# Kernel optimization log

Measured on AMD Instinct MI355X. Metric: run time of the kernel, lower is better.

The kernel has to match this reference:

```python
import jax, jax.numpy as jnp
import numpy as np

N, E = 20000, 320000          # nodes, edges (avg degree 16)
IN, OUT, EC = 256, 256, 64    # in_channels == out_channels (required by BN placement)
BN_EPS = 1e-5


def setup_inputs() -> dict:
    key = jax.random.key(0)
    ks = jax.random.split(key, 8)
    def lin(k, fan_in, fan_out):
        # kaiming-uniform-ish init like nn.Linear
        bound = 1.0 / np.sqrt(fan_in)
        return jax.random.uniform(k, (fan_in, fan_out), jnp.float32, -bound, bound)
    return {
        "x": jax.random.normal(ks[0], (N, IN), jnp.float32),
        "edge_index": jax.random.randint(ks[1], (2, E), 0, N),
        "edge_attr": jax.random.normal(ks[2], (E, EC), jnp.float32),
        "W_edge": lin(ks[3], EC, IN),          # edge_lin (no bias)
        "W_rel": lin(ks[4], IN, OUT),           # GraphConv lin_rel weight
        "b_rel": jnp.zeros((OUT,), jnp.float32),  # GraphConv lin_rel bias
        "W_root": lin(ks[5], IN, OUT),          # GraphConv lin_root (no bias)
        "gamma": jnp.ones((OUT,), jnp.float32),  # BN weight
        "beta": jnp.zeros((OUT,), jnp.float32),  # BN bias
        "W_res": lin(ks[6], IN, OUT),           # res_lin (no bias)
    }


def reference(x, edge_index, edge_attr, W_edge, W_rel, b_rel, W_root, gamma, beta, W_res):
    src, dst = edge_index[0], edge_index[1]
    # edge feature projection: [E, EC] -> [E, IN]
    e = edge_attr @ W_edge
    # message passing: gather source node feats, modulate by edge feats, scatter-add to dst
    msg = x[src] * e                                   # [E, IN]
    agg = jax.ops.segment_sum(msg, dst, num_segments=x.shape[0])  # [N, IN]
    # GraphConv: lin_rel(aggregate) + lin_root(x)
    h = agg @ W_rel + b_rel + x @ W_root               # [N, OUT]
    h = jax.nn.relu(h)
    # BatchNorm1d (training mode: batch statistics over nodes)
    mean = h.mean(axis=0)
    var = ((h - mean) ** 2).mean(axis=0)
    h = (h - mean) * jax.lax.rsqrt(var + BN_EPS) * gamma + beta
    # residual branch
    return h + x @ W_res
```

## Files before the change

kernel.cpp:

```cpp
#include <hip/hip_runtime.h>
#include <hip/hip_bf16.h>


#define N_NODES 20000
#define E_EDGES 320000
#define C 256
#define CE 64
#define MAXDEG 64
#define BN_EPS 1e-5f

typedef __attribute__((ext_vector_type(8))) short short8;
typedef __attribute__((ext_vector_type(8))) unsigned short ushort8;
typedef __attribute__((ext_vector_type(4))) float f32x4;
typedef __attribute__((ext_vector_type(4))) unsigned short ushort4v;

static __device__ __forceinline__ float bf2f(unsigned short u) {
    union { unsigned int i; float f; } v; v.i = (unsigned int)u << 16; return v.f;
}
static __device__ __forceinline__ unsigned short f2bf(float f) {
    __hip_bfloat16 h = __float2bfloat16(f);
    return *reinterpret_cast<unsigned short*>(&h);
}

__global__ __launch_bounds__(256) void k_wprep(
    const float* __restrict__ W_rel, const float* __restrict__ W_root,
    const float* __restrict__ W_res, const float* __restrict__ W_edge,
    unsigned short* __restrict__ wt_hi, unsigned short* __restrict__ wte_hi) {
    int b = blockIdx.x, n = threadIdx.x;
    if (b < 768) {
        int m = b >> 8, k = b & 255;
        const float* W = (m == 0) ? W_rel : (m == 1) ? W_root : W_res;
        size_t o = (((size_t)m * 16 + (n >> 4)) * 8 + (k >> 5)) * 512
                 + (size_t)(((n & 15) | (((k >> 3) & 3) << 4)) * 8) + (k & 7);
        wt_hi[o] = f2bf(W[k * C + n]);
    } else {
        int k = b - 768;
        size_t o = ((size_t)(n >> 4) * 2 + (k >> 5)) * 512
                 + (size_t)(((n & 15) | (((k >> 3) & 3) << 4)) * 8) + (k & 7);
        wte_hi[o] = f2bf(W_edge[k * C + n]);
    }
}

__global__ void k_bucket(const int* __restrict__ ei, int* __restrict__ deg,
                         int2* __restrict__ elist2) {
    int e = blockIdx.x * blockDim.x + threadIdx.x;
    if (e < E_EDGES) {
        int d = ei[E_EDGES + e];
        int s = ei[e];
        int slot = atomicAdd(&deg[d], 1);
        if (slot < MAXDEG) elist2[d * MAXDEG + slot] = make_int2(e, s);
    }
}

__global__ __launch_bounds__(256, 4) void k_fusedagg(
    const float* __restrict__ x, const float* __restrict__ ea,
    const unsigned short* __restrict__ wte_hi,
    const int* __restrict__ deg, const int2* __restrict__ elist2,
    float* __restrict__ agg) {
    __shared__ short lds[16384];
    __shared__ int es[MAXDEG], ss[MAXDEG];
    const int tid = threadIdx.x;
    const int node = blockIdx.x;

    int dr = deg[node];
    const int d = dr < MAXDEG ? dr : MAXDEG;
    if (d == 0) {
        agg[(size_t)node * C + tid] = 0.f;
        return;
    }
    if (tid < d) {
        int2 p = elist2[node * MAXDEG + tid];
        es[tid] = p.x; ss[tid] = p.y;
    }
    __syncthreads();

    const int rtmax = (d + 15) >> 4;

#pragma unroll
    for (int i = 0; i < 4; ++i) {
        int f = tid + 256 * i;
        int r = f >> 4, k4 = (f & 15) * 4;
        if (r < rtmax * 16) {
            float4 v = {0.f, 0.f, 0.f, 0.f};
            if (r < d)
                v = *reinterpret_cast<const float4*>(&ea[(size_t)es[r] * CE + k4]);
            unsigned short h0 = f2bf(v.x), h1 = f2bf(v.y), h2 = f2bf(v.z), h3 = f2bf(v.w);
            ushort4v hv = {h0, h1, h2, h3};
            ushort4v lv = {f2bf(v.x - bf2f(h0)), f2bf(v.y - bf2f(h1)),
                           f2bf(v.z - bf2f(h2)), f2bf(v.w - bf2f(h3))};
            int rt = r >> 4, ks = k4 >> 5;
            int lane = (r & 15) | (((k4 >> 3) & 3) << 4);
            int base = (((rt * 2 + ks) * 2 + 0) * 64 + lane) * 8 + (k4 & 7);
            *reinterpret_cast<ushort4v*>(&lds[base]) = hv;
            *reinterpret_cast<ushort4v*>(&lds[base + 512]) = lv;
        }
    }
    __syncthreads();

    const int w = tid >> 6, l = tid & 63;
    f32x4 acc[2][4];
#pragma unroll
    for (int rt = 0; rt < 2; ++rt)
#pragma unroll
        for (int ct = 0; ct < 4; ++ct) acc[rt][ct] = (f32x4){0.f, 0.f, 0.f, 0.f};
    const int rtc = rtmax < 2 ? rtmax : 2;

#pragma unroll
    for (int ks = 0; ks < 2; ++ks) {
        short8 b[4];
#pragma unroll
        for (int ct = 0; ct < 4; ++ct) {
            int nt = w * 4 + ct;
            b[ct] = *reinterpret_cast<const short8*>(&wte_hi[(size_t)(nt * 2 + ks) * 512 + l * 8]);
        }
        for (int rt = 0; rt < rtc; ++rt) {
            int base = ((rt * 2 + ks) * 2) * 512 + l * 8;
            short8 ah = *reinterpret_cast<const short8*>(&lds[base]);
            short8 al = *reinterpret_cast<const short8*>(&lds[base + 512]);
#pragma unroll
            for (int ct = 0; ct < 4; ++ct) {
                acc[rt][ct] = __builtin_amdgcn_mfma_f32_16x16x32_bf16(ah, b[ct], acc[rt][ct], 0, 0, 0);
                acc[rt][ct] = __builtin_amdgcn_mfma_f32_16x16x32_bf16(al, b[ct], acc[rt][ct], 0, 0, 0);
            }
        }
    }

    f32x4 acc3[2][4];
    const bool deep = (rtmax > 2);
    if (deep) {
#pragma unroll
        for (int rt = 0; rt < 2; ++rt)
#pragma unroll
            for (int ct = 0; ct < 4; ++ct) acc3[rt][ct] = (f32x4){0.f, 0.f, 0.f, 0.f};
#pragma unroll
        for (int ks = 0; ks < 2; ++ks) {
            short8 b[4];
#pragma unroll
            for (int ct = 0; ct < 4; ++ct) {
                int nt = w * 4 + ct;
                b[ct] = *reinterpret_cast<const short8*>(&wte_hi[(size_t)(nt * 2 + ks) * 512 + l * 8]);
            }
            for (int rt = 2; rt < rtmax; ++rt) {
                int base = ((rt * 2 + ks) * 2) * 512 + l * 8;
                short8 ah = *reinterpret_cast<const short8*>(&lds[base]);
                short8 al = *reinterpret_cast<const short8*>(&lds[base + 512]);
#pragma unroll
                for (int ct = 0; ct < 4; ++ct) {
                    acc3[rt - 2][ct] = __builtin_amdgcn_mfma_f32_16x16x32_bf16(ah, b[ct], acc3[rt - 2][ct], 0, 0, 0);
                    acc3[rt - 2][ct] = __builtin_amdgcn_mfma_f32_16x16x32_bf16(al, b[ct], acc3[rt - 2][ct], 0, 0, 0);
                }
            }
        }
    }

    __syncthreads();
    for (int rt = 0; rt < rtc; ++rt)
#pragma unroll
        for (int ct = 0; ct < 4; ++ct) {
            int col = w * 64 + ct * 16 + (l & 15);
#pragma unroll
            for (int q = 0; q < 4; ++q) {
                int r = rt * 16 + (l >> 4) * 4 + q;
                lds[r * C + col] = (short)f2bf(acc[rt][ct][q]);
            }
        }
    if (deep) {
        for (int rt = 2; rt < rtmax; ++rt)
#pragma unroll
            for (int ct = 0; ct < 4; ++ct) {
                int col = w * 64 + ct * 16 + (l & 15);
#pragma unroll
                for (int q = 0; q < 4; ++q) {
                    int r = rt * 16 + (l >> 4) * 4 + q;
                    lds[r * C + col] = (short)f2bf(acc3[rt - 2][ct][q]);
                }
            }
    }
    __syncthreads();

    const int c = tid;
    float accv = 0.f;
    for (int i = 0; i < d; i += 4) {
        int m = d - i;
        float xv[4], ev[4];
#pragma unroll
        for (int j = 0; j < 4; ++j) {
            if (j < m) {
                xv[j] = x[(size_t)ss[i + j] * C + c];
                ev[j] = bf2f((unsigned short)lds[(i + j) * C + c]);
            } else { xv[j] = 0.f; ev[j] = 0.f; }
        }
#pragma unroll
        for (int j = 0; j < 4; ++j) accv += ev[j] * xv[j];
    }
    agg[(size_t)node * C + c] = accv;
}

__global__ __launch_bounds__(256, 4) void k_gemm(
    const float* __restrict__ aggt, const float* __restrict__ x,
    const unsigned short* __restrict__ wt_hi,
    float* __restrict__ g_rel, float* __restrict__ g_root,
    float* __restrict__ g_res) {
    __shared__ short AB[16384];
    const int tid = threadIdx.x;
    const int n0 = blockIdx.x * 32;
    const int mat = blockIdx.y;
    const float* Asrc = (mat == 0) ? aggt : x;
    float* dst = (mat == 0) ? g_rel : (mat == 1) ? g_root : g_res;

#pragma unroll
    for (int i = 0; i < 8; ++i) {
        int f = tid + 256 * i;
        int r = f >> 6, k4 = (f & 63) * 4;
        float4 v = *reinterpret_cast<const float4*>(&Asrc[(size_t)(n0 + r) * C + k4]);
        unsigned short h0 = f2bf(v.x), h1 = f2bf(v.y), h2 = f2bf(v.z), h3 = f2bf(v.w);
        ushort4v hv = {h0, h1, h2, h3};
        ushort4v lv = {f2bf(v.x - bf2f(h0)), f2bf(v.y - bf2f(h1)),
                       f2bf(v.z - bf2f(h2)), f2bf(v.w - bf2f(h3))};
        int rt = r >> 4, ks = k4 >> 5;
        int lane = (r & 15) | (((k4 >> 3) & 3) << 4);
        int base = (((rt * 8 + ks) * 2 + 0) * 64 + lane) * 8 + (k4 & 7);
        *reinterpret_cast<ushort4v*>(&AB[base]) = hv;
        *reinterpret_cast<ushort4v*>(&AB[base + 512]) = lv;
    }
    __syncthreads();

    const int w = tid >> 6, l = tid & 63;
    f32x4 acc[2][4];
#pragma unroll
    for (int rt = 0; rt < 2; ++rt)
#pragma unroll
        for (int ct = 0; ct < 4; ++ct) acc[rt][ct] = (f32x4){0.f, 0.f, 0.f, 0.f};

    const unsigned short* wbase = wt_hi + (size_t)mat * 16 * 8 * 512;

#pragma unroll
    for (int ks = 0; ks < 8; ++ks) {
        short8 b[4];
#pragma unroll
        for (int ct = 0; ct < 4; ++ct) {
            int nt = w * 4 + ct;
            b[ct] = *reinterpret_cast<const short8*>(&wbase[(size_t)(nt * 8 + ks) * 512 + l * 8]);
        }
        short8 ah[2], al[2];
#pragma unroll
        for (int rt = 0; rt < 2; ++rt) {
            int base = ((rt * 8 + ks) * 2) * 512 + l * 8;
            ah[rt] = *reinterpret_cast<const short8*>(&AB[base]);
            al[rt] = *reinterpret_cast<const short8*>(&AB[base + 512]);
        }
#pragma unroll
        for (int ct = 0; ct < 4; ++ct)
#pragma unroll
            for (int rt = 0; rt < 2; ++rt) {
                acc[rt][ct] = __builtin_amdgcn_mfma_f32_16x16x32_bf16(ah[rt], b[ct], acc[rt][ct], 0, 0, 0);
                acc[rt][ct] = __builtin_amdgcn_mfma_f32_16x16x32_bf16(al[rt], b[ct], acc[rt][ct], 0, 0, 0);
            }
    }

#pragma unroll
    for (int ct = 0; ct < 4; ++ct) {
        int col = w * 64 + ct * 16 + (l & 15);
#pragma unroll
        for (int rt = 0; rt < 2; ++rt)
#pragma unroll
            for (int q = 0; q < 4; ++q) {
                int node = n0 + rt * 16 + (l >> 4) * 4 + q;
                dst[(size_t)node * C + col] = acc[rt][ct][q];
            }
    }
}

__global__ __launch_bounds__(256) void k_bnstat(
    const float* __restrict__ g_rel, const float* __restrict__ g_root,
    const float* __restrict__ b_rel, float* __restrict__ chsum,
    float* __restrict__ chsumsq) {
    __shared__ float2 red[4 * 256];
    const int tid = threadIdx.x;
    const int c0 = (tid & 63) * 4, rg = tid >> 6;
    const int base = blockIdx.x * 32;
    float4 b4 = *reinterpret_cast<const float4*>(&b_rel[c0]);
    float4 s1 = {0.f, 0.f, 0.f, 0.f}, s2 = {0.f, 0.f, 0.f, 0.f};
#pragma unroll
    for (int i = 0; i < 8; ++i) {
        size_t row = (size_t)(base + rg * 8 + i) * C + c0;
        float4 hr = *reinterpret_cast<const float4*>(&g_rel[row]);
        float4 ho = *reinterpret_cast<const float4*>(&g_root[row]);
        float4 h;
        h.x = fmaxf(hr.x + ho.x + b4.x, 0.f);
        h.y = fmaxf(hr.y + ho.y + b4.y, 0.f);
        h.z = fmaxf(hr.z + ho.z + b4.z, 0.f);
        h.w = fmaxf(hr.w + ho.w + b4.w, 0.f);
        s1.x += h.x; s1.y += h.y; s1.z += h.z; s1.w += h.w;
        s2.x += h.x * h.x; s2.y += h.y * h.y;
        s2.z += h.z * h.z; s2.w += h.w * h.w;
    }
    red[rg * 256 + c0 + 0] = make_float2(s1.x, s2.x);
    red[rg * 256 + c0 + 1] = make_float2(s1.y, s2.y);
    red[rg * 256 + c0 + 2] = make_float2(s1.z, s2.z);
    red[rg * 256 + c0 + 3] = make_float2(s1.w, s2.w);
    __syncthreads();
    float a = 0.f, bsum = 0.f;
#pragma unroll
    for (int g = 0; g < 4; ++g) {
        float2 v = red[g * 256 + tid];
        a += v.x; bsum += v.y;
    }
    atomicAdd(&chsum[tid], a);
    atomicAdd(&chsumsq[tid], bsum);
}

__global__ __launch_bounds__(256) void k_finalize(
    const float* __restrict__ g_rel, const float* __restrict__ g_root,
    const float* __restrict__ b_rel, const float* __restrict__ chsum,
    const float* __restrict__ chsumsq, const float* __restrict__ gamma,
    const float* __restrict__ beta, float* out) {
    const float invN = 1.f / (float)N_NODES;
    int i = (blockIdx.x * blockDim.x + threadIdx.x) * 4;
    if (i >= N_NODES * C) return;
    int c = i & (C - 1);
    float4 hr = *reinterpret_cast<const float4*>(&g_rel[i]);
    float4 ho = *reinterpret_cast<const float4*>(&g_root[i]);
    float4 b4 = *reinterpret_cast<const float4*>(&b_rel[c]);
    float4 rv = *reinterpret_cast<const float4*>(&out[i]);
    float4 o;
    {
        float h = fmaxf(hr.x + ho.x + b4.x, 0.f);
        float m = chsum[c + 0] * invN;
        float v = chsumsq[c + 0] * invN - m * m;
        o.x = (h - m) * rsqrtf(v + BN_EPS) * gamma[c + 0] + beta[c + 0] + rv.x;
    }
    {
        float h = fmaxf(hr.y + ho.y + b4.y, 0.f);
        float m = chsum[c + 1] * invN;
        float v = chsumsq[c + 1] * invN - m * m;
        o.y = (h - m) * rsqrtf(v + BN_EPS) * gamma[c + 1] + beta[c + 1] + rv.y;
    }
    {
        float h = fmaxf(hr.z + ho.z + b4.z, 0.f);
        float m = chsum[c + 2] * invN;
        float v = chsumsq[c + 2] * invN - m * m;
        o.z = (h - m) * rsqrtf(v + BN_EPS) * gamma[c + 2] + beta[c + 2] + rv.z;
    }
    {
        float h = fmaxf(hr.w + ho.w + b4.w, 0.f);
        float m = chsum[c + 3] * invN;
        float v = chsumsq[c + 3] * invN - m * m;
        o.w = (h - m) * rsqrtf(v + BN_EPS) * gamma[c + 3] + beta[c + 3] + rv.w;
    }
    *reinterpret_cast<float4*>(&out[i]) = o;
}

extern "C" void kernel_launch(void* const* d_in, const int* in_sizes, int n_in,
                              void* d_out, int out_size, void* d_ws, size_t ws_size,
                              hipStream_t stream) {
    const float* x      = (const float*)d_in[0];
    const int*   ei     = (const int*)  d_in[1];
    const float* ea     = (const float*)d_in[2];
    const float* W_edge = (const float*)d_in[3];
    const float* W_rel  = (const float*)d_in[4];
    const float* b_rel  = (const float*)d_in[5];
    const float* W_root = (const float*)d_in[6];
    const float* gamma  = (const float*)d_in[7];
    const float* beta   = (const float*)d_in[8];
    const float* W_res  = (const float*)d_in[9];
    float* out = (float*)d_out;

    float* ws      = (float*)d_ws;
    float* aggt    = ws;
    float* chsum   = ws + (size_t)N_NODES * C;
    float* chsumsq = chsum + C;
    int*   deg     = (int*)(chsumsq + C);
    int2*  elist2  = (int2*)(deg + N_NODES);
    float* g_rel   = (float*)(elist2 + (size_t)N_NODES * MAXDEG);
    float* g_root  = g_rel + (size_t)N_NODES * C;
    unsigned short* wte_hi = (unsigned short*)(g_root + (size_t)N_NODES * C);
    unsigned short* wt_hi  = wte_hi + C * CE;
    size_t need = (char*)(wt_hi + 3 * C * C) - (char*)d_ws;
    if (ws_size < need) return;

    hipMemsetAsync(chsum, 0, 2 * C * sizeof(float) + N_NODES * sizeof(int), stream);

    k_wprep<<<832, 256, 0, stream>>>(W_rel, W_root, W_res, W_edge, wt_hi, wte_hi);
    k_bucket<<<(E_EDGES + 255) / 256, 256, 0, stream>>>(ei, deg, elist2);
    k_fusedagg<<<N_NODES, 256, 0, stream>>>(x, ea, wte_hi, deg, elist2, aggt);
    k_gemm<<<dim3(N_NODES / 32, 3), 256, 0, stream>>>(aggt, x, wt_hi,
                                                      g_rel, g_root, out);
    k_bnstat<<<N_NODES / 32, 256, 0, stream>>>(g_rel, g_root, b_rel, chsum, chsumsq);
    k_finalize<<<(N_NODES * C / 4 + 255) / 256, 256, 0, stream>>>(
        g_rel, g_root, b_rel, chsum, chsumsq, gamma, beta, out);
}
```

Before: 354.3 us.

## Pack two destination nodes per block in fused aggregation and swizzle LDS

The fused edge-projection/aggregation kernel now handles two destination nodes per block. Their edge lists are concatenated into one MFMA tile when the combined degree fits in 64 rows, otherwise the nodes are processed in two passes. This fills more of each 16-row MFMA tile, which previously held about one node's 16 edges, and halves the block count. It also XOR-swizzles the bf16 edge-feature staging buffer in LDS to reduce bank conflicts, at the cost of extra syncs and branching per pass.

```diff
diff --git a/kernel.cpp b/kernel.cpp
--- a/kernel.cpp
+++ b/kernel.cpp
@@ -60,78 +60,58 @@
     __shared__ short lds[16384];
     __shared__ int es[MAXDEG], ss[MAXDEG];
     const int tid = threadIdx.x;
-    const int node = blockIdx.x;
-
-    int dr = deg[node];
-    const int d = dr < MAXDEG ? dr : MAXDEG;
-    if (d == 0) {
-        agg[(size_t)node * C + tid] = 0.f;
-        return;
-    }
-    if (tid < d) {
-        int2 p = elist2[node * MAXDEG + tid];
-        es[tid] = p.x; ss[tid] = p.y;
-    }
-    __syncthreads();
-
-    const int rtmax = (d + 15) >> 4;
-
-#pragma unroll
-    for (int i = 0; i < 4; ++i) {
-        int f = tid + 256 * i;
-        int r = f >> 4, k4 = (f & 15) * 4;
-        if (r < rtmax * 16) {
-            float4 v = {0.f, 0.f, 0.f, 0.f};
-            if (r < d)
-                v = *reinterpret_cast<const float4*>(&ea[(size_t)es[r] * CE + k4]);
-            unsigned short h0 = f2bf(v.x), h1 = f2bf(v.y), h2 = f2bf(v.z), h3 = f2bf(v.w);
-            ushort4v hv = {h0, h1, h2, h3};
-            ushort4v lv = {f2bf(v.x - bf2f(h0)), f2bf(v.y - bf2f(h1)),
-                           f2bf(v.z - bf2f(h2)), f2bf(v.w - bf2f(h3))};
-            int rt = r >> 4, ks = k4 >> 5;
-            int lane = (r & 15) | (((k4 >> 3) & 3) << 4);
-            int base = (((rt * 2 + ks) * 2 + 0) * 64 + lane) * 8 + (k4 & 7);
-            *reinterpret_cast<ushort4v*>(&lds[base]) = hv;
-            *reinterpret_cast<ushort4v*>(&lds[base + 512]) = lv;
-        }
-    }
-    __syncthreads();
-
-    const int w = tid >> 6, l = tid & 63;
-    f32x4 acc[2][4];
-#pragma unroll
-    for (int rt = 0; rt < 2; ++rt)
-#pragma unroll
-        for (int ct = 0; ct < 4; ++ct) acc[rt][ct] = (f32x4){0.f, 0.f, 0.f, 0.f};
-    const int rtc = rtmax < 2 ? rtmax : 2;
-
-#pragma unroll
-    for (int ks = 0; ks < 2; ++ks) {
-        short8 b[4];
-#pragma unroll
-        for (int ct = 0; ct < 4; ++ct) {
-            int nt = w * 4 + ct;
-            b[ct] = *reinterpret_cast<const short8*>(&wte_hi[(size_t)(nt * 2 + ks) * 512 + l * 8]);
-        }
-        for (int rt = 0; rt < rtc; ++rt) {
-            int base = ((rt * 2 + ks) * 2) * 512 + l * 8;
-            short8 ah = *reinterpret_cast<const short8*>(&lds[base]);
-            short8 al = *reinterpret_cast<const short8*>(&lds[base + 512]);
-#pragma unroll
-            for (int ct = 0; ct < 4; ++ct) {
-                acc[rt][ct] = __builtin_amdgcn_mfma_f32_16x16x32_bf16(ah, b[ct], acc[rt][ct], 0, 0, 0);
-                acc[rt][ct] = __builtin_amdgcn_mfma_f32_16x16x32_bf16(al, b[ct], acc[rt][ct], 0, 0, 0);
-            }
-        }
-    }
-
-    f32x4 acc3[2][4];
-    const bool deep = (rtmax > 2);
-    if (deep) {
+    const int n0 = blockIdx.x * 2, n1 = n0 + 1;
+
+    int d0r = deg[n0], d1r = deg[n1];
+    const int d0 = d0r < MAXDEG ? d0r : MAXDEG;
+    const int d1 = d1r < MAXDEG ? d1r : MAXDEG;
+    const int passes = (d0 + d1 <= MAXDEG) ? 1 : 2;
+
+    for (int pass = 0; pass < passes; ++pass) {
+        int R, bnd, nA, nB;
+        if (passes == 1) { R = d0 + d1; bnd = d0; nA = n0; nB = n1; }
+        else if (pass == 0) { R = d0; bnd = d0; nA = n0; nB = -1; }
+        else { R = d1; bnd = d1; nA = n1; nB = -1; }
+
+        if (tid < R) {
+            int node = (tid < bnd) ? nA : nB;
+            int slot = (tid < bnd) ? tid : tid - bnd;
+            int2 p = elist2[node * MAXDEG + slot];
+            es[tid] = p.x; ss[tid] = p.y;
+        }
+        __syncthreads();
+
+        const int rtmax = (R + 15) >> 4;
+
+#pragma unroll
+        for (int i = 0; i < 4; ++i) {
+            int f = tid + 256 * i;
+            int r = f >> 4, k4 = (f & 15) * 4;
+            if (r < rtmax * 16) {
+                float4 v = {0.f, 0.f, 0.f, 0.f};
+                if (r < R)
+                    v = *reinterpret_cast<const float4*>(&ea[(size_t)es[r] * CE + k4]);
+                unsigned short h0 = f2bf(v.x), h1 = f2bf(v.y), h2 = f2bf(v.z), h3 = f2bf(v.w);
+                ushort4v hv = {h0, h1, h2, h3};
+                ushort4v lv = {f2bf(v.x - bf2f(h0)), f2bf(v.y - bf2f(h1)),
+                               f2bf(v.z - bf2f(h2)), f2bf(v.w - bf2f(h3))};
+                int rt = r >> 4, ks = k4 >> 5;
+                int lane = (r & 15) | (((k4 >> 3) & 3) << 4);
+                int base = (((rt * 2 + ks) * 2 + 0) * 64 + lane) * 8 + (k4 & 7);
+                *reinterpret_cast<ushort4v*>(&lds[base]) = hv;
+                *reinterpret_cast<ushort4v*>(&lds[base + 512]) = lv;
+            }
+        }
+        __syncthreads();
+
+        const int w = tid >> 6, l = tid & 63;
+        f32x4 acc[2][4];
 #pragma unroll
         for (int rt = 0; rt < 2; ++rt)
 #pragma unroll
-            for (int ct = 0; ct < 4; ++ct) acc3[rt][ct] = (f32x4){0.f, 0.f, 0.f, 0.f};
+            for (int ct = 0; ct < 4; ++ct) acc[rt][ct] = (f32x4){0.f, 0.f, 0.f, 0.f};
+        const int rtc = rtmax < 2 ? rtmax : 2;
+
 #pragma unroll
         for (int ks = 0; ks < 2; ++ks) {
             short8 b[4];
@@ -140,60 +120,110 @@
                 int nt = w * 4 + ct;
                 b[ct] = *reinterpret_cast<const short8*>(&wte_hi[(size_t)(nt * 2 + ks) * 512 + l * 8]);
             }
-            for (int rt = 2; rt < rtmax; ++rt) {
+            for (int rt = 0; rt < rtc; ++rt) {
                 int base = ((rt * 2 + ks) * 2) * 512 + l * 8;
                 short8 ah = *reinterpret_cast<const short8*>(&lds[base]);
                 short8 al = *reinterpret_cast<const short8*>(&lds[base + 512]);
 #pragma unroll
                 for (int ct = 0; ct < 4; ++ct) {
-                    acc3[rt - 2][ct] = __builtin_amdgcn_mfma_f32_16x16x32_bf16(ah, b[ct], acc3[rt - 2][ct], 0, 0, 0);
-                    acc3[rt - 2][ct] = __builtin_amdgcn_mfma_f32_16x16x32_bf16(al, b[ct], acc3[rt - 2][ct], 0, 0, 0);
+                    acc[rt][ct] = __builtin_amdgcn_mfma_f32_16x16x32_bf16(ah, b[ct], acc[rt][ct], 0, 0, 0);
+                    acc[rt][ct] = __builtin_amdgcn_mfma_f32_16x16x32_bf16(al, b[ct], acc[rt][ct], 0, 0, 0);
                 }
             }
         }
-    }
-
-    __syncthreads();
-    for (int rt = 0; rt < rtc; ++rt)
-#pragma unroll
-        for (int ct = 0; ct < 4; ++ct) {
-            int col = w * 64 + ct * 16 + (l & 15);
-#pragma unroll
-            for (int q = 0; q < 4; ++q) {
-                int r = rt * 16 + (l >> 4) * 4 + q;
-                lds[r * C + col] = (short)f2bf(acc[rt][ct][q]);
-            }
-        }
-    if (deep) {
-        for (int rt = 2; rt < rtmax; ++rt)
+
+        f32x4 acc3[2][4];
+        const bool deep = (rtmax > 2);
+        if (deep) {
+#pragma unroll
+            for (int rt = 0; rt < 2; ++rt)
+#pragma unroll
+                for (int ct = 0; ct < 4; ++ct) acc3[rt][ct] = (f32x4){0.f, 0.f, 0.f, 0.f};
+#pragma unroll
+            for (int ks = 0; ks < 2; ++ks) {
+                short8 b[4];
+#pragma unroll
+                for (int ct = 0; ct < 4; ++ct) {
+                    int nt = w * 4 + ct;
+                    b[ct] = *reinterpret_cast<const short8*>(&wte_hi[(size_t)(nt * 2 + ks) * 512 + l * 8]);
+                }
+                for (int rt = 2; rt < rtmax; ++rt) {
+                    int base = ((rt * 2 + ks) * 2) * 512 + l * 8;
+                    short8 ah = *reinterpret_cast<const short8*>(&lds[base]);
+                    short8 al = *reinterpret_cast<const short8*>(&lds[base + 512]);
+#pragma unroll
+                    for (int ct = 0; ct < 4; ++ct) {
+                        acc3[rt - 2][ct] = __builtin_amdgcn_mfma_f32_16x16x32_bf16(ah, b[ct], acc3[rt - 2][ct], 0, 0, 0);
+                        acc3[rt - 2][ct] = __builtin_amdgcn_mfma_f32_16x16x32_bf16(al, b[ct], acc3[rt - 2][ct], 0, 0, 0);
+                    }
+                }
+            }
+        }
+
+        __syncthreads();
+        char* ldsb = reinterpret_cast<char*>(lds);
+        for (int rt = 0; rt < rtc; ++rt)
 #pragma unroll
             for (int ct = 0; ct < 4; ++ct) {
                 int col = w * 64 + ct * 16 + (l & 15);
 #pragma unroll
                 for (int q = 0; q < 4; ++q) {
                     int r = rt * 16 + (l >> 4) * 4 + q;
-                    lds[r * C + col] = (short)f2bf(acc3[rt - 2][ct][q]);
+                    int byte = ((r * C + col) * 2) ^ ((r & 7) << 4);
+                    *reinterpret_cast<short*>(ldsb + byte) = (short)f2bf(acc[rt][ct][q]);
                 }
             }
-    }
-    __syncthreads();
-
-    const int c = tid;
-    float accv = 0.f;
-    for (int i = 0; i < d; i += 4) {
-        int m = d - i;
-        float xv[4], ev[4];
-#pragma unroll
-        for (int j = 0; j < 4; ++j) {
-            if (j < m) {
-                xv[j] = x[(size_t)ss[i + j] * C + c];
-                ev[j] = bf2f((unsigned short)lds[(i + j) * C + c]);
-            } else { xv[j] = 0.f; ev[j] = 0.f; }
-        }
-#pragma unroll
-        for (int j = 0; j < 4; ++j) accv += ev[j] * xv[j];
-    }
-    agg[(size_t)node * C + c] = accv;
+        if (deep) {
+            for (int rt = 2; rt < rtmax; ++rt)
+#pragma unroll
+                for (int ct = 0; ct < 4; ++ct) {
+                    int col = w * 64 + ct * 16 + (l & 15);
+#pragma unroll
+                    for (int q = 0; q < 4; ++q) {
+                        int r = rt * 16 + (l >> 4) * 4 + q;
+                        int byte = ((r * C + col) * 2) ^ ((r & 7) << 4);
+                        *reinterpret_cast<short*>(ldsb + byte) = (short)f2bf(acc3[rt - 2][ct][q]);
+                    }
+                }
+        }
+        __syncthreads();
+
+        const int c = tid;
+        float accA = 0.f, accB = 0.f;
+        for (int i = 0; i < bnd; i += 4) {
+            int m = bnd - i;
+            float xv[4], ev[4];
+#pragma unroll
+            for (int j = 0; j < 4; ++j) {
+                if (j < m) {
+                    int r = i + j;
+                    xv[j] = x[(size_t)ss[r] * C + c];
+                    int byte = ((r * C + c) * 2) ^ ((r & 7) << 4);
+                    ev[j] = bf2f(*reinterpret_cast<const unsigned short*>(ldsb + byte));
+                } else { xv[j] = 0.f; ev[j] = 0.f; }
+            }
+#pragma unroll
+            for (int j = 0; j < 4; ++j) accA += ev[j] * xv[j];
+        }
+        for (int i = bnd; i < R; i += 4) {
+            int m = R - i;
+            float xv[4], ev[4];
+#pragma unroll
+            for (int j = 0; j < 4; ++j) {
+                if (j < m) {
+                    int r = i + j;
+                    xv[j] = x[(size_t)ss[r] * C + c];
+                    int byte = ((r * C + c) * 2) ^ ((r & 7) << 4);
+                    ev[j] = bf2f(*reinterpret_cast<const unsigned short*>(ldsb + byte));
+                } else { xv[j] = 0.f; ev[j] = 0.f; }
+            }
+#pragma unroll
+            for (int j = 0; j < 4; ++j) accB += ev[j] * xv[j];
+        }
+        agg[(size_t)nA * C + c] = accA;
+        if (nB >= 0) agg[(size_t)nB * C + c] = accB;
+        __syncthreads();
+    }
 }
 
 __global__ __launch_bounds__(256, 4) void k_gemm(
@@ -383,7 +413,7 @@
 
     k_wprep<<<832, 256, 0, stream>>>(W_rel, W_root, W_res, W_edge, wt_hi, wte_hi);
     k_bucket<<<(E_EDGES + 255) / 256, 256, 0, stream>>>(ei, deg, elist2);
-    k_fusedagg<<<N_NODES, 256, 0, stream>>>(x, ea, wte_hi, deg, elist2, aggt);
+    k_fusedagg<<<N_NODES / 2, 256, 0, stream>>>(x, ea, wte_hi, deg, elist2, aggt);
     k_gemm<<<dim3(N_NODES / 32, 3), 256, 0, stream>>>(aggt, x, wt_hi,
                                                       g_rel, g_root, out);
     k_bnstat<<<N_NODES / 32, 256, 0, stream>>>(g_rel, g_root, b_rel, chsum, chsumsq);
```

After: 391.3 us. +10.4%, slower.
